# Kernel optimization log

Measured on AMD Instinct MI355X. Metric: run time of the kernel, lower is better.

## Reference

```python
import jax, jax.numpy as jnp
import numpy as np

E = 262144      # total neighbor edges across all (sample, timestep) pairs
B = 1024        # samples with non-zero history
L = 10          # seq_len
T = B * L       # total timesteps (segments)
H = 128         # h_dim
N_ENT = 40000
N_REL = 256


def setup_inputs() -> dict:
    key = jax.random.key(0)
    ks = jax.random.split(key, 16)
    return {
        "nbr_ent": jax.random.randint(ks[0], (E,), 0, N_ENT),
        "nbr_rel": jax.random.randint(ks[1], (E,), 0, N_REL),
        "nbr_att": jax.random.uniform(ks[2], (E,), dtype=jnp.float32),
        "seg_ids": jnp.sort(jax.random.randint(ks[3], (E,), 0, T)),
        "self_att": jax.random.uniform(ks[4], (B, L), dtype=jnp.float32),
        "s_ids": jax.random.randint(ks[5], (B,), 0, N_ENT),
        "r_ids": jax.random.randint(ks[6], (B,), 0, N_REL),
        "ent_embeds": jax.random.normal(ks[7], (N_ENT, H), dtype=jnp.float32),
        "rel_embeds": jax.random.normal(ks[8], (N_REL, H), dtype=jnp.float32),
        "W1_w": jax.random.normal(ks[9], (H, 1), dtype=jnp.float32) * 0.1,
        "W1_b": jax.random.normal(ks[10], (H,), dtype=jnp.float32) * 0.1,
        "W3_w": jax.random.normal(ks[11], (H, 3 * H), dtype=jnp.float32) * 0.05,
        "W3_b": jax.random.normal(ks[12], (H,), dtype=jnp.float32) * 0.05,
        "W4_w": jax.random.normal(ks[13], (H, 2 * H), dtype=jnp.float32) * 0.05,
        "W4_b": jax.random.normal(ks[14], (H,), dtype=jnp.float32) * 0.05,
    }


def reference(nbr_ent, nbr_rel, nbr_att, seg_ids, self_att, s_ids, r_ids,
              ent_embeds, rel_embeds, W1_w, W1_b, W3_w, W3_b, W4_w, W4_b):
    # --- per-edge embeddings (the body of get_sorted_s_r_embed) ---
    # W1: scalar attribute -> h_dim, then ReLU
    e_att = jax.nn.relu(nbr_att[:, None] * W1_w[:, 0][None, :] + W1_b)   # [E, H]
    e_s = ent_embeds[nbr_ent]                                            # [E, H]
    e_r = rel_embeds[nbr_rel]                                            # [E, H]
    e = jax.nn.relu(jnp.concatenate([e_att, e_s, e_r], -1) @ W3_w.T + W3_b)      # [E, H]
    e_static = jax.nn.relu(jnp.concatenate([e_s, e_r], -1) @ W4_w.T + W4_b)      # [E, H]

    # --- sparse-mask segment mean (torch.sparse.mm with 0/1 mask / len_s) ---
    counts = jax.ops.segment_sum(jnp.ones_like(nbr_att), seg_ids, num_segments=T)
    denom = jnp.maximum(counts, 1.0)[:, None]                            # guard empty segments
    embeds_mean = jax.ops.segment_sum(e, seg_ids, num_segments=T) / denom          # [T, H]
    embeds_static_mean = jax.ops.segment_sum(e_static, seg_ids, num_segments=T) / denom

    embeds_mean = embeds_mean.reshape(B, L, H)
    embeds_static_mean = embeds_static_mean.reshape(B, L, H)

    # --- per-sample fill of padded sequence tensors ---
    self_att_emb = jax.nn.relu(self_att[..., None] * W1_w[:, 0] + W1_b)  # [B, L, H]
    self_e = jnp.broadcast_to(ent_embeds[s_ids][:, None, :], (B, L, H))  # repeat over time
    self_r = jnp.broadcast_to(rel_embeds[r_ids][:, None, :], (B, L, H))

    s_embed_seq = jnp.concatenate([self_e, self_r, embeds_static_mean], -1)   # [B, L, 3H]
    att_embed_seq = jnp.concatenate([self_att_emb, self_e, embeds_mean], -1)  # [B, L, 3H]
    # dropout omitted (eval mode); pack_padded_sequence returns padded tensors here
    return s_embed_seq, att_embed_seq
```

## Files before the change

### kernel.cpp

```cpp
#include <hip/hip_runtime.h>
#include <hip/hip_bf16.h>

#define E_EDGES 262144
#define B_SAMP  1024
#define L_SEQ   10
#define T_SEG   (B_SAMP * L_SEQ)
#define H_DIM   128
#define N_ENT_C 40000
#define N_REL_C 256

typedef __attribute__((ext_vector_type(8))) short short8;
typedef __attribute__((ext_vector_type(4))) float f32x4;

__device__ __forceinline__ float b2f(__hip_bfloat16 x) { return __bfloat162float(x); }
__device__ __forceinline__ unsigned short f2bu(float x) {
    return __bfloat16_as_ushort(__float2bfloat16(x));
}
__device__ __forceinline__ float bu2f(unsigned short u) {
    return b2f(__ushort_as_bfloat16(u));
}

__device__ __forceinline__ float loadF(const void* base, int idx, int isB16) {
    if (isB16) return b2f(((const __hip_bfloat16*)base)[idx]);
    return ((const float*)base)[idx];
}
__device__ __forceinline__ int loadI(const void* base, int idx, int is64) {
    if (is64) return (int)(((const long long*)base)[idx]);
    return ((const int*)base)[idx];
}

__global__ void k1_prep(const void* __restrict__ att_raw,
                        const void* __restrict__ sid_raw,
                        const void* __restrict__ W1w, const void* __restrict__ W1b,
                        const void* __restrict__ W3b, const void* __restrict__ W4b,
                        int* __restrict__ flag, int* __restrict__ iflag,
                        float* __restrict__ W1w_f, float* __restrict__ W1b_f,
                        float* __restrict__ W3b_f, float* __restrict__ W4b_f,
                        float* __restrict__ bpts, int* __restrict__ pnIn)
{
    __shared__ int cF, cI, sF;
    __shared__ float thr[128];
    const int tid = threadIdx.x;
    if (tid == 0) { cF = 0; cI = 0; }
    __syncthreads();

    const unsigned short* pa = (const unsigned short*)att_raw;
    int c = 0;
    for (int i = tid; i < 2048; i += 256) if (pa[i] <= 0x3F80u) c++;
    atomicAdd(&cF, c);
    const int* ps = (const int*)sid_raw;
    c = 0;
    for (int i = tid; i < 512; i += 256) if (ps[2 * i + 1] == 0) c++;
    atomicAdd(&cI, c);
    __syncthreads();
    if (tid == 0) {
        sF = (cF >= 1900) ? 1 : 0;
        *flag = sF;
        *iflag = (cI >= 256) ? 1 : 0;
    }
    __syncthreads();
    const int isB = sF;

    if (tid < 128) {
        float w = loadF(W1w, tid, isB);
        float b = loadF(W1b, tid, isB);
        W1w_f[tid] = w; W1b_f[tid] = b;
        W3b_f[tid] = loadF(W3b, tid, isB);
        W4b_f[tid] = loadF(W4b, tid, isB);
        float t = 2.0f;
        if (w != 0.0f) {
            float tt = -b / w;
            if (tt > 0.0f && tt < 1.0f) t = tt;
        }
        thr[tid] = t;
    }
    __syncthreads();
    for (int ph = 0; ph < 128; ++ph) {
        int i = 2 * tid + (ph & 1);
        if (tid < 64 && i + 1 < 128) {
            float a0 = thr[i], a1 = thr[i + 1];
            if (a0 > a1) { thr[i] = a1; thr[i + 1] = a0; }
        }
        __syncthreads();
    }
    if (tid < 128) bpts[tid] = thr[tid];
    if (tid == 0) {
        int n = 0;
        for (int i = 0; i < 128; ++i) if (thr[i] < 1.5f) n++;
        *pnIn = n;
    }
}

__global__ void __launch_bounds__(256)
k2_tables(const void* __restrict__ W3w, const void* __restrict__ W4w,
          const void* __restrict__ seg_ids,
          const int* __restrict__ flag, const int* __restrict__ iflag,
          const float* __restrict__ W1w_f, const float* __restrict__ W1b_f,
          const float* __restrict__ bpts, const int* __restrict__ pnIn,
          unsigned short* __restrict__ wctEb, unsigned short* __restrict__ wctRb,
          float2* __restrict__ ab3, int* __restrict__ starts)
{
    const int bid = blockIdx.x, tid = threadIdx.x;
    const int isB = *flag;
    if (bid < 256) {
        int gid = bid * 256 + tid;
        if (gid < 32768) {
            int n = gid >> 7, k = gid & 127;
            float v = (n < 128) ? loadF(W3w, n * 384 + 128 + k, isB)
                                : loadF(W4w, (n - 128) * 256 + k, isB);
            wctEb[gid] = f2bu(v);
        } else {
            int j = gid - 32768;
            int n = j >> 7, k = j & 127;
            float v = (n < 128) ? loadF(W3w, n * 384 + 256 + k, isB)
                                : loadF(W4w, (n - 128) * 256 + 128 + k, isB);
            wctRb[j] = f2bu(v);
        }
    } else if (bid < 321) {
        __shared__ float w1s[128], b1s[128];
        const int h = tid & 127;
        if (tid < 128) { w1s[tid] = W1w_f[tid]; b1s[tid] = W1b_f[tid]; }
        __syncthreads();
        const int nIn = *pnIn;
        const int j = (bid - 256) * 2 + (tid >> 7);
        if (j <= nIn) {
            float left  = (j == 0)   ? 0.0f : bpts[j - 1];
            float right = (j == nIn) ? 1.0f : bpts[j];
            float mid = 0.5f * (left + right);
            float a = 0.0f, b = 0.0f;
            for (int k = 0; k < 128; ++k) {
                if (fmaf(mid, w1s[k], b1s[k]) > 0.0f) {
                    float w3 = loadF(W3w, h * 384 + k, isB);
                    a = fmaf(w1s[k], w3, a);
                    b = fmaf(b1s[k], w3, b);
                }
            }
            ab3[j * 128 + h] = make_float2(a, b);
        }
    } else {
        int t = (bid - 321) * 256 + tid;
        if (t <= T_SEG) {
            const int i64 = *iflag;
            int lo = 0, hi = E_EDGES;
            while (lo < hi) {
                int m = (lo + hi) >> 1;
                if (loadI(seg_ids, m, i64) < t) lo = m + 1; else hi = m;
            }
            starts[t] = lo;
        }
    }
}

__global__ void __launch_bounds__(256)
k3_gemm(const void* __restrict__ ent_raw, const void* __restrict__ rel_raw,
        const int* __restrict__ flag,
        const unsigned short* __restrict__ wctEb,
        const unsigned short* __restrict__ wctRb,
        unsigned int* __restrict__ entp2, unsigned int* __restrict__ relp2)
{
    const int isB = *flag;
    const int gw = blockIdx.x * 4 + (threadIdx.x >> 6);
    const int lane = threadIdx.x & 63;
    const int quad = lane >> 4, l16 = lane & 15;

    const void* A; const unsigned short* WT; unsigned int* out;
    int mtile, npair;
    if (gw < (N_ENT_C / 16) * 8) {
        A = ent_raw; WT = wctEb; out = entp2;
        mtile = gw >> 3; npair = gw & 7;
    } else {
        int g = gw - (N_ENT_C / 16) * 8;
        if (g >= (N_REL_C / 16) * 8) return;
        A = rel_raw; WT = wctRb; out = relp2;
        mtile = g >> 3; npair = g & 7;
    }

    const int mrow = mtile * 16 + l16;
    const int n3 = npair * 16 + l16;
    f32x4 acc3 = {0.f, 0.f, 0.f, 0.f}, acc4 = {0.f, 0.f, 0.f, 0.f};
    #pragma unroll
    for (int kk = 0; kk < 4; ++kk) {
        const int kb = kk * 32 + quad * 8;
        short8 av;
        if (isB) {
            av = *(const short8*)((const short*)A + mrow * 128 + kb);
        } else {
            const float* pa = (const float*)A + mrow * 128 + kb;
            float4 f0 = *(const float4*)pa;
            float4 f1 = *(const float4*)(pa + 4);
            av[0] = (short)f2bu(f0.x); av[1] = (short)f2bu(f0.y);
            av[2] = (short)f2bu(f0.z); av[3] = (short)f2bu(f0.w);
            av[4] = (short)f2bu(f1.x); av[5] = (short)f2bu(f1.y);
            av[6] = (short)f2bu(f1.z); av[7] = (short)f2bu(f1.w);
        }
        short8 bv3 = *(const short8*)((const short*)WT + n3 * 128 + kb);
        short8 bv4 = *(const short8*)((const short*)WT + (n3 + 128) * 128 + kb);
        acc3 = __builtin_amdgcn_mfma_f32_16x16x32_bf16(av, bv3, acc3, 0, 0, 0);
        acc4 = __builtin_amdgcn_mfma_f32_16x16x32_bf16(av, bv4, acc4, 0, 0, 0);
    }
    #pragma unroll
    for (int r = 0; r < 4; ++r) {
        int m = mtile * 16 + quad * 4 + r;
        int h = npair * 16 + l16;
        unsigned int w = (unsigned int)f2bu(acc3[r])
                       | ((unsigned int)f2bu(acc4[r]) << 16);
        out[m * 128 + h] = w;
    }
}

__global__ void __launch_bounds__(128)
k4_segment(const void* __restrict__ nbr_ent, const void* __restrict__ nbr_rel,
           const void* __restrict__ att_raw,
           const int* __restrict__ starts,
           const unsigned int* __restrict__ entp2,
           const unsigned int* __restrict__ relp2,
           const float2* __restrict__ ab3,
           const float* __restrict__ bpts_g, const int* __restrict__ pnIn,
           const float* __restrict__ W3b_f, const float* __restrict__ W4b_f,
           const void* __restrict__ sat_raw,
           const void* __restrict__ s_ids, const void* __restrict__ r_ids,
           const void* __restrict__ ent_raw, const void* __restrict__ rel_raw,
           const float* __restrict__ W1w_f, const float* __restrict__ W1b_f,
           const int* __restrict__ flag, const int* __restrict__ iflag,
           float* __restrict__ outS, float* __restrict__ outA)
{
    const int t = blockIdx.x, h = threadIdx.x;
    const int isB = *flag, i64 = *iflag;
    const int s = starts[t], e = starts[t + 1];

    __shared__ float bptsS[128];
    __shared__ int entS[128], relS[128], jS[128];
    __shared__ float attS[128];
    bptsS[h] = bpts_g[h];
    const int nIn = *pnIn;

    const float b3h = W3b_f[h], b4h = W4b_f[h];
    float acc3 = 0.0f, acc4 = 0.0f;

    for (int base = s; base < e; base += 128) {
        const int n = min(128, e - base);
        __syncthreads();
        if (h < n) {
            const int i = base + h;
            entS[h] = loadI(nbr_ent, i, i64);
            relS[h] = loadI(nbr_rel, i, i64);
            float att = loadF(att_raw, i, isB);
            attS[h] = att;
            int lo = 0, hi = nIn;
            while (lo < hi) {
                int m = (lo + hi) >> 1;
                if (bptsS[m] <= att) lo = m + 1; else hi = m;
            }
            jS[h] = lo;
        }
        __syncthreads();
        for (int ii = 0; ii < n; ++ii) {
            const int ent = entS[ii], rel = relS[ii], j = jS[ii];
            const float att = attS[ii];
            unsigned int ew = entp2[ent * 128 + h];
            unsigned int rw = relp2[rel * 128 + h];
            float2 ab = ab3[j * 128 + h];
            float p3s = bu2f((unsigned short)(ew & 0xFFFFu));
            float p4s = bu2f((unsigned short)(ew >> 16));
            float p3r = bu2f((unsigned short)(rw & 0xFFFFu));
            float p4r = bu2f((unsigned short)(rw >> 16));
            float z3 = fmaf(att, ab.x, ab.y) + p3s + p3r + b3h;
            float z4 = p4s + p4r + b4h;
            acc3 += fmaxf(z3, 0.0f);
            acc4 += fmaxf(z4, 0.0f);
        }
    }

    const int cnt = e - s;
    const float inv = (cnt > 0) ? (1.0f / (float)cnt) : 1.0f;
    const int b = t / L_SEQ;
    const int sid = loadI(s_ids, b, i64);
    const int rid = loadI(r_ids, b, i64);
    const float se = loadF(ent_raw, sid * 128 + h, isB);
    const float sr = loadF(rel_raw, rid * 128 + h, isB);
    const float sa = loadF(sat_raw, t, isB);
    const float sae = fmaxf(fmaf(sa, W1w_f[h], W1b_f[h]), 0.0f);

    const size_t bs = (size_t)t * 384;
    outS[bs + h]       = se;
    outS[bs + 128 + h] = sr;
    outS[bs + 256 + h] = acc4 * inv;
    outA[bs + h]       = sae;
    outA[bs + 128 + h] = se;
    outA[bs + 256 + h] = acc3 * inv;
}

extern "C" void kernel_launch(void* const* d_in, const int* in_sizes, int n_in,
                              void* d_out, int out_size, void* d_ws, size_t ws_size,
                              hipStream_t stream)
{
    const void* nbr_ent = d_in[0];
    const void* nbr_rel = d_in[1];
    const void* nbr_att = d_in[2];
    const void* seg_ids = d_in[3];
    const void* self_att = d_in[4];
    const void* s_ids = d_in[5];
    const void* r_ids = d_in[6];
    const void* ent_embeds = d_in[7];
    const void* rel_embeds = d_in[8];
    const void* W1w = d_in[9];
    const void* W1b = d_in[10];
    const void* W3w = d_in[11];
    const void* W3b = d_in[12];
    const void* W4w = d_in[13];
    const void* W4b = d_in[14];

    char* ws = (char*)d_ws;
    size_t off = 0;
    auto alloc = [&](size_t bytes) -> void* {
        void* p = ws + off;
        off = (off + bytes + 255) & ~(size_t)255;
        return p;
    };
    int*   flag   = (int*)alloc(4);
    int*   iflag  = (int*)alloc(4);
    int*   pnIn   = (int*)alloc(4);
    float* W1w_f  = (float*)alloc(128 * 4);
    float* W1b_f  = (float*)alloc(128 * 4);
    float* W3b_f  = (float*)alloc(128 * 4);
    float* W4b_f  = (float*)alloc(128 * 4);
    float* bpts   = (float*)alloc(128 * 4);
    int*   starts = (int*)alloc((T_SEG + 1) * 4);
    unsigned short* wctEb = (unsigned short*)alloc(256 * 128 * 2);
    unsigned short* wctRb = (unsigned short*)alloc(256 * 128 * 2);
    float2* ab3   = (float2*)alloc(129 * 128 * 8);
    unsigned int* entp2 = (unsigned int*)alloc((size_t)N_ENT_C * 128 * 4);
    unsigned int* relp2 = (unsigned int*)alloc((size_t)N_REL_C * 128 * 4);

    float* outS = (float*)d_out;
    float* outA = outS + (size_t)T_SEG * 384;

    k1_prep<<<1, 256, 0, stream>>>(nbr_att, s_ids, W1w, W1b, W3b, W4b,
                                   flag, iflag, W1w_f, W1b_f, W3b_f, W4b_f,
                                   bpts, pnIn);

    k2_tables<<<362, 256, 0, stream>>>(W3w, W4w, seg_ids, flag, iflag,
                                       W1w_f, W1b_f, bpts, pnIn,
                                       wctEb, wctRb, ab3, starts);

    {
        int waves = (N_ENT_C / 16) * 8 + (N_REL_C / 16) * 8;
        k3_gemm<<<(waves + 3) / 4, 256, 0, stream>>>(
            ent_embeds, rel_embeds, flag, wctEb, wctRb, entp2, relp2);
    }

    k4_segment<<<T_SEG, 128, 0, stream>>>(
        nbr_ent, nbr_rel, nbr_att, starts, entp2, relp2, ab3, bpts, pnIn,
        W3b_f, W4b_f, self_att, s_ids, r_ids, ent_embeds, rel_embeds,
        W1w_f, W1b_f, flag, iflag, outS, outA);
}
```

Baseline: 216.0 us.

## Merge prep kernels and tile entity GEMM with LDS-staged rows per block

Result: faster. 189.8 us (-12.1%).

```diff
diff --git a/kernel.cpp b/kernel.cpp
--- a/kernel.cpp
+++ b/kernel.cpp
@@ -29,79 +29,43 @@
     return ((const int*)base)[idx];
 }
 
-__global__ void k1_prep(const void* __restrict__ att_raw,
-                        const void* __restrict__ sid_raw,
-                        const void* __restrict__ W1w, const void* __restrict__ W1b,
-                        const void* __restrict__ W3b, const void* __restrict__ W4b,
-                        int* __restrict__ flag, int* __restrict__ iflag,
-                        float* __restrict__ W1w_f, float* __restrict__ W1b_f,
-                        float* __restrict__ W3b_f, float* __restrict__ W4b_f,
-                        float* __restrict__ bpts, int* __restrict__ pnIn)
-{
-    __shared__ int cF, cI, sF;
-    __shared__ float thr[128];
-    const int tid = threadIdx.x;
+__device__ __forceinline__ void detect_dtypes(const void* att_raw,
+                                              const void* sid_raw,
+                                              int tid, int& isB, int& i64)
+{
+    __shared__ int cF, cI;
     if (tid == 0) { cF = 0; cI = 0; }
     __syncthreads();
-
     const unsigned short* pa = (const unsigned short*)att_raw;
     int c = 0;
     for (int i = tid; i < 2048; i += 256) if (pa[i] <= 0x3F80u) c++;
-    atomicAdd(&cF, c);
+    if (c) atomicAdd(&cF, c);
     const int* ps = (const int*)sid_raw;
     c = 0;
     for (int i = tid; i < 512; i += 256) if (ps[2 * i + 1] == 0) c++;
-    atomicAdd(&cI, c);
+    if (c) atomicAdd(&cI, c);
     __syncthreads();
-    if (tid == 0) {
-        sF = (cF >= 1900) ? 1 : 0;
-        *flag = sF;
-        *iflag = (cI >= 256) ? 1 : 0;
-    }
-    __syncthreads();
-    const int isB = sF;
-
-    if (tid < 128) {
-        float w = loadF(W1w, tid, isB);
-        float b = loadF(W1b, tid, isB);
-        W1w_f[tid] = w; W1b_f[tid] = b;
-        W3b_f[tid] = loadF(W3b, tid, isB);
-        W4b_f[tid] = loadF(W4b, tid, isB);
-        float t = 2.0f;
-        if (w != 0.0f) {
-            float tt = -b / w;
-            if (tt > 0.0f && tt < 1.0f) t = tt;
-        }
-        thr[tid] = t;
-    }
-    __syncthreads();
-    for (int ph = 0; ph < 128; ++ph) {
-        int i = 2 * tid + (ph & 1);
-        if (tid < 64 && i + 1 < 128) {
-            float a0 = thr[i], a1 = thr[i + 1];
-            if (a0 > a1) { thr[i] = a1; thr[i + 1] = a0; }
-        }
-        __syncthreads();
-    }
-    if (tid < 128) bpts[tid] = thr[tid];
-    if (tid == 0) {
-        int n = 0;
-        for (int i = 0; i < 128; ++i) if (thr[i] < 1.5f) n++;
-        *pnIn = n;
-    }
+    isB = (cF >= 1900) ? 1 : 0;
+    i64 = (cI >= 256) ? 1 : 0;
 }
 
 __global__ void __launch_bounds__(256)
-k2_tables(const void* __restrict__ W3w, const void* __restrict__ W4w,
-          const void* __restrict__ seg_ids,
-          const int* __restrict__ flag, const int* __restrict__ iflag,
-          const float* __restrict__ W1w_f, const float* __restrict__ W1b_f,
-          const float* __restrict__ bpts, const int* __restrict__ pnIn,
-          unsigned short* __restrict__ wctEb, unsigned short* __restrict__ wctRb,
-          float2* __restrict__ ab3, int* __restrict__ starts)
+ka_prep(const void* __restrict__ W3w, const void* __restrict__ W4w,
+        const void* __restrict__ W1w, const void* __restrict__ W1b,
+        const void* __restrict__ W3b, const void* __restrict__ W4b,
+        const void* __restrict__ seg_ids,
+        const void* __restrict__ att_raw, const void* __restrict__ sid_raw,
+        unsigned short* __restrict__ wctEb, unsigned short* __restrict__ wctRb,
+        float2* __restrict__ ab3, int* __restrict__ starts,
+        float* __restrict__ W1w_f, float* __restrict__ W1b_f,
+        float* __restrict__ W3b_f, float* __restrict__ W4b_f,
+        float* __restrict__ bpts, int* __restrict__ pnIn,
+        int* __restrict__ flag, int* __restrict__ iflag)
 {
     const int bid = blockIdx.x, tid = threadIdx.x;
-    const int isB = *flag;
+    int isB, i64;
+    detect_dtypes(att_raw, sid_raw, tid, isB, i64);
+
     if (bid < 256) {
         int gid = bid * 256 + tid;
         if (gid < 32768) {
@@ -116,16 +80,59 @@
                                 : loadF(W4w, (n - 128) * 256 + 128 + k, isB);
             wctRb[j] = f2bu(v);
         }
-    } else if (bid < 321) {
-        __shared__ float w1s[128], b1s[128];
+        return;
+    }
+
+    if (bid < 321 || bid == 362) {
+        __shared__ float w1s[128], b1s[128], srt[128];
+        __shared__ int nInS;
+        if (tid < 128) {
+            float w = loadF(W1w, tid, isB);
+            float b = loadF(W1b, tid, isB);
+            w1s[tid] = w; b1s[tid] = b;
+        }
+        __syncthreads();
+        if (tid < 128) {
+            float w = w1s[tid], b = b1s[tid];
+            float t = 2.0f;
+            if (w != 0.0f) {
+                float tt = -b / w;
+                if (tt > 0.0f && tt < 1.0f) t = tt;
+            }
+            srt[tid] = t;
+        }
+        __syncthreads();
+        float myt = 0.0f; int rank = 0, n = 0;
+        if (tid < 128) {
+            myt = srt[tid];
+            for (int j = 0; j < 128; ++j) {
+                float v = srt[j];
+                rank += (v < myt) || (v == myt && j < tid);
+                n += (v < 1.5f);
+            }
+        }
+        __syncthreads();
+        if (tid < 128) srt[rank] = myt;
+        if (tid == 0) nInS = n;
+        __syncthreads();
+        const int nIn = nInS;
+
+        if (bid == 362) {
+            if (tid < 128) {
+                W1w_f[tid] = w1s[tid];
+                W1b_f[tid] = b1s[tid];
+                W3b_f[tid] = loadF(W3b, tid, isB);
+                W4b_f[tid] = loadF(W4b, tid, isB);
+                bpts[tid] = srt[tid];
+            }
+            if (tid == 0) { *pnIn = nIn; *flag = isB; *iflag = i64; }
+            return;
+        }
+        const int j = (bid - 256) * 2 + (tid >> 7);
         const int h = tid & 127;
-        if (tid < 128) { w1s[tid] = W1w_f[tid]; b1s[tid] = W1b_f[tid]; }
-        __syncthreads();
-        const int nIn = *pnIn;
-        const int j = (bid - 256) * 2 + (tid >> 7);
         if (j <= nIn) {
-            float left  = (j == 0)   ? 0.0f : bpts[j - 1];
-            float right = (j == nIn) ? 1.0f : bpts[j];
+            float left  = (j == 0)   ? 0.0f : srt[j - 1];
+            float right = (j == nIn) ? 1.0f : srt[j];
             float mid = 0.5f * (left + right);
             float a = 0.0f, b = 0.0f;
             for (int k = 0; k < 128; ++k) {
@@ -137,79 +144,95 @@
             }
             ab3[j * 128 + h] = make_float2(a, b);
         }
-    } else {
-        int t = (bid - 321) * 256 + tid;
-        if (t <= T_SEG) {
-            const int i64 = *iflag;
-            int lo = 0, hi = E_EDGES;
-            while (lo < hi) {
-                int m = (lo + hi) >> 1;
-                if (loadI(seg_ids, m, i64) < t) lo = m + 1; else hi = m;
-            }
-            starts[t] = lo;
-        }
-    }
-}
+        return;
+    }
+
+    int t = (bid - 321) * 256 + tid;
+    if (t <= T_SEG) {
+        int lo = 0, hi = E_EDGES;
+        while (lo < hi) {
+            int m = (lo + hi) >> 1;
+            if (loadI(seg_ids, m, i64) < t) lo = m + 1; else hi = m;
+        }
+        starts[t] = lo;
+    }
+}
+
+#define KB_ENT_BLOCKS (N_ENT_C / 64)
+#define KB_REL_BLOCKS (N_REL_C / 64)
 
 __global__ void __launch_bounds__(256)
-k3_gemm(const void* __restrict__ ent_raw, const void* __restrict__ rel_raw,
+kb_gemm(const void* __restrict__ ent_raw, const void* __restrict__ rel_raw,
         const int* __restrict__ flag,
         const unsigned short* __restrict__ wctEb,
         const unsigned short* __restrict__ wctRb,
         unsigned int* __restrict__ entp2, unsigned int* __restrict__ relp2)
 {
     const int isB = *flag;
-    const int gw = blockIdx.x * 4 + (threadIdx.x >> 6);
-    const int lane = threadIdx.x & 63;
+    const int bid = blockIdx.x, tid = threadIdx.x;
+
+    const void* A; const unsigned short* WT; unsigned int* out; int m0;
+    if (bid < KB_ENT_BLOCKS) { A = ent_raw; WT = wctEb; out = entp2; m0 = bid * 64; }
+    else { A = rel_raw; WT = wctRb; out = relp2; m0 = (bid - KB_ENT_BLOCKS) * 64; }
+
+    __shared__ unsigned short As[64][136];
+
+    if (isB) {
+        for (int v = tid; v < 1024; v += 256) {
+            int e = v * 8, r = e >> 7, cc = e & 127;
+            short8 x = *(const short8*)((const short*)A + m0 * 128 + e);
+            *(short8*)&As[r][cc] = x;
+        }
+    } else {
+        for (int v = tid; v < 2048; v += 256) {
+            int e = v * 4, r = e >> 7, cc = e & 127;
+            float4 f = *(const float4*)((const float*)A + m0 * 128 + e);
+            unsigned int lo = (unsigned int)f2bu(f.x) | ((unsigned int)f2bu(f.y) << 16);
+            unsigned int hi = (unsigned int)f2bu(f.z) | ((unsigned int)f2bu(f.w) << 16);
+            *(uint2*)&As[r][cc] = make_uint2(lo, hi);
+        }
+    }
+    __syncthreads();
+
+    const int wave = tid >> 6, lane = tid & 63;
     const int quad = lane >> 4, l16 = lane & 15;
 
-    const void* A; const unsigned short* WT; unsigned int* out;
-    int mtile, npair;
-    if (gw < (N_ENT_C / 16) * 8) {
-        A = ent_raw; WT = wctEb; out = entp2;
-        mtile = gw >> 3; npair = gw & 7;
-    } else {
-        int g = gw - (N_ENT_C / 16) * 8;
-        if (g >= (N_REL_C / 16) * 8) return;
-        A = rel_raw; WT = wctRb; out = relp2;
-        mtile = g >> 3; npair = g & 7;
-    }
-
-    const int mrow = mtile * 16 + l16;
-    const int n3 = npair * 16 + l16;
-    f32x4 acc3 = {0.f, 0.f, 0.f, 0.f}, acc4 = {0.f, 0.f, 0.f, 0.f};
+    f32x4 acc3[8], acc4[8];
+    #pragma unroll
+    for (int np = 0; np < 8; ++np) {
+        acc3[np] = (f32x4){0.f, 0.f, 0.f, 0.f};
+        acc4[np] = (f32x4){0.f, 0.f, 0.f, 0.f};
+    }
+
     #pragma unroll
     for (int kk = 0; kk < 4; ++kk) {
         const int kb = kk * 32 + quad * 8;
-        short8 av;
-        if (isB) {
-            av = *(const short8*)((const short*)A + mrow * 128 + kb);
-        } else {
-            const float* pa = (const float*)A + mrow * 128 + kb;
-            float4 f0 = *(const float4*)pa;
-            float4 f1 = *(const float4*)(pa + 4);
-            av[0] = (short)f2bu(f0.x); av[1] = (short)f2bu(f0.y);
-            av[2] = (short)f2bu(f0.z); av[3] = (short)f2bu(f0.w);
-            av[4] = (short)f2bu(f1.x); av[5] = (short)f2bu(f1.y);
-            av[6] = (short)f2bu(f1.z); av[7] = (short)f2bu(f1.w);
-        }
-        short8 bv3 = *(const short8*)((const short*)WT + n3 * 128 + kb);
-        short8 bv4 = *(const short8*)((const short*)WT + (n3 + 128) * 128 + kb);
-        acc3 = __builtin_amdgcn_mfma_f32_16x16x32_bf16(av, bv3, acc3, 0, 0, 0);
-        acc4 = __builtin_amdgcn_mfma_f32_16x16x32_bf16(av, bv4, acc4, 0, 0, 0);
-    }
+        short8 av = *(const short8*)&As[wave * 16 + l16][kb];
+        #pragma unroll
+        for (int np = 0; np < 8; ++np) {
+            const short* bp = (const short*)WT + (np * 16 + l16) * 128 + kb;
+            short8 bv3 = *(const short8*)bp;
+            short8 bv4 = *(const short8*)(bp + 128 * 128);
+            acc3[np] = __builtin_amdgcn_mfma_f32_16x16x32_bf16(av, bv3, acc3[np], 0, 0, 0);
+            acc4[np] = __builtin_amdgcn_mfma_f32_16x16x32_bf16(av, bv4, acc4[np], 0, 0, 0);
+        }
+    }
+
     #pragma unroll
-    for (int r = 0; r < 4; ++r) {
-        int m = mtile * 16 + quad * 4 + r;
-        int h = npair * 16 + l16;
-        unsigned int w = (unsigned int)f2bu(acc3[r])
-                       | ((unsigned int)f2bu(acc4[r]) << 16);
-        out[m * 128 + h] = w;
+    for (int np = 0; np < 8; ++np) {
+        #pragma unroll
+        for (int r = 0; r < 4; ++r) {
+            int m = m0 + wave * 16 + quad * 4 + r;
+            int h = np * 16 + l16;
+            unsigned int w = (unsigned int)f2bu(acc3[np][r])
+                           | ((unsigned int)f2bu(acc4[np][r]) << 16);
+            out[m * 128 + h] = w;
+        }
     }
 }
 
 __global__ void __launch_bounds__(128)
-k4_segment(const void* __restrict__ nbr_ent, const void* __restrict__ nbr_rel,
+kc_segment(const void* __restrict__ nbr_ent, const void* __restrict__ nbr_rel,
            const void* __restrict__ att_raw,
            const int* __restrict__ starts,
            const unsigned int* __restrict__ entp2,
@@ -335,21 +358,16 @@
     float* outS = (float*)d_out;
     float* outA = outS + (size_t)T_SEG * 384;
 
-    k1_prep<<<1, 256, 0, stream>>>(nbr_att, s_ids, W1w, W1b, W3b, W4b,
-                                   flag, iflag, W1w_f, W1b_f, W3b_f, W4b_f,
-                                   bpts, pnIn);
-
-    k2_tables<<<362, 256, 0, stream>>>(W3w, W4w, seg_ids, flag, iflag,
-                                       W1w_f, W1b_f, bpts, pnIn,
-                                       wctEb, wctRb, ab3, starts);
-
-    {
-        int waves = (N_ENT_C / 16) * 8 + (N_REL_C / 16) * 8;
-        k3_gemm<<<(waves + 3) / 4, 256, 0, stream>>>(
-            ent_embeds, rel_embeds, flag, wctEb, wctRb, entp2, relp2);
-    }
-
-    k4_segment<<<T_SEG, 128, 0, stream>>>(
+    ka_prep<<<363, 256, 0, stream>>>(W3w, W4w, W1w, W1b, W3b, W4b,
+                                     seg_ids, nbr_att, s_ids,
+                                     wctEb, wctRb, ab3, starts,
+                                     W1w_f, W1b_f, W3b_f, W4b_f,
+                                     bpts, pnIn, flag, iflag);
+
+    kb_gemm<<<KB_ENT_BLOCKS + KB_REL_BLOCKS, 256, 0, stream>>>(
+        ent_embeds, rel_embeds, flag, wctEb, wctRb, entp2, relp2);
+
+    kc_segment<<<T_SEG, 128, 0, stream>>>(
         nbr_ent, nbr_rel, nbr_att, starts, entp2, relp2, ab3, bpts, pnIn,
         W3b_f, W4b_f, self_att, s_ids, r_ids, ent_embeds, rel_embeds,
         W1w_f, W1b_f, flag, iflag, outS, outA);
```
